# Optimization experiments

Hardware: AMD Instinct MI355X
Metric: run time of the kernel (lower is better)

## Reference

```python
import jax, jax.numpy as jnp
import numpy as np

N_NODES = 50000
N_EDGES = 800000
N_GRAPHS = 512
F_IN = 16
E_DIM = 64
D = 128          # encoder_dim
L_DIM = 64       # latent_dim
MP_STEPS = 3
S2S_STEPS = 3
NEG_SLOPE = 0.01


def _leaky(v):
    return jax.nn.leaky_relu(v, NEG_SLOPE)


def setup_inputs() -> dict:
    key = jax.random.key(0)
    ks = jax.random.split(key, 24)

    def w(k, fan_in, shape):
        return jax.random.normal(k, shape, jnp.float32) / np.sqrt(fan_in)

    inp = {
        "x": jax.random.normal(ks[0], (N_NODES, F_IN), jnp.float32),
        "edge_index": jax.random.randint(ks[1], (2, N_EDGES), 0, N_NODES, jnp.int64),
        "edge_attr": jax.random.normal(ks[2], (N_EDGES, 4), jnp.float32),
        "batch": jnp.sort(jax.random.randint(ks[3], (N_NODES,), 0, N_GRAPHS, jnp.int64)),
        # embedding: Linear(F_IN -> E_DIM); weights stored [in, out]
        "W_emb": w(ks[4], F_IN, (F_IN, E_DIM)),
        "b_emb": jnp.zeros((E_DIM,), jnp.float32),
        # first: Linear(E_DIM -> D)
        "W_first": w(ks[5], E_DIM, (E_DIM, D)),
        "b_first": jnp.zeros((D,), jnp.float32),
        # SAGEConv: lin_l (aggregated neighbors, with bias), lin_r (root, no bias)
        "W_l": w(ks[6], D, (D, D)),
        "b_l": jnp.zeros((D,), jnp.float32),
        "W_r": w(ks[7], D, (D, D)),
        # GRU (1 layer): gates ordered r,z,n as in torch
        "gru_Wih": w(ks[8], D, (D, 3 * D)),
        "gru_Whh": w(ks[9], D, (D, 3 * D)),
        "gru_bih": jnp.zeros((3 * D,), jnp.float32),
        "gru_bhh": jnp.zeros((3 * D,), jnp.float32),
        # Set2Set LSTM: input 2D -> hidden D; gates ordered i,f,g,o as in torch
        "lstm_Wih": w(ks[10], 2 * D, (2 * D, 4 * D)),
        "lstm_Whh": w(ks[11], D, (D, 4 * D)),
        "lstm_bih": jnp.zeros((4 * D,), jnp.float32),
        "lstm_bhh": jnp.zeros((4 * D,), jnp.float32),
        # linear: Linear(2D -> D), final: Linear(D -> L_DIM)
        "W_lin": w(ks[12], 2 * D, (2 * D, D)),
        "b_lin": jnp.zeros((D,), jnp.float32),
        "W_fin": w(ks[13], D, (D, L_DIM)),
        "b_fin": jnp.zeros((L_DIM,), jnp.float32),
    }
    return inp


def _gru_step(x, h, Wih, Whh, bih, bhh):
    gi = x @ Wih + bih
    gh = h @ Whh + bhh
    ir, iz, inn = jnp.split(gi, 3, axis=-1)
    hr, hz, hn = jnp.split(gh, 3, axis=-1)
    r = jax.nn.sigmoid(ir + hr)
    z = jax.nn.sigmoid(iz + hz)
    n = jnp.tanh(inn + r * hn)
    return (1.0 - z) * n + z * h


def _lstm_step(x, h, c, Wih, Whh, bih, bhh):
    g = x @ Wih + bih + h @ Whh + bhh
    i, f, gg, o = jnp.split(g, 4, axis=-1)
    c_new = jax.nn.sigmoid(f) * c + jax.nn.sigmoid(i) * jnp.tanh(gg)
    h_new = jax.nn.sigmoid(o) * jnp.tanh(c_new)
    return h_new, c_new


def reference(x, edge_index, edge_attr, batch,
              W_emb, b_emb, W_first, b_first,
              W_l, b_l, W_r,
              gru_Wih, gru_Whh, gru_bih, gru_bhh,
              lstm_Wih, lstm_Whh, lstm_bih, lstm_bhh,
              W_lin, b_lin, W_fin, b_fin):
    # edge_attr is ignored (PyG SAGEConv does not use it).
    out = _leaky(x @ W_emb + b_emb)        # [N, E_DIM]
    out = _leaky(out @ W_first + b_first)  # [N, D]
    h = out                                # GRU hidden state [N, D]
    src, dst = edge_index[0], edge_index[1]
    for _ in range(MP_STEPS):
        agg = jax.ops.segment_sum(out[src], dst, num_segments=N_NODES)  # [N, D]
        m = jax.nn.relu(agg @ W_l + b_l + out @ W_r)  # SAGEConv(aggr='add') + root
        out = _gru_step(m, h, gru_Wih, gru_Whh, gru_bih, gru_bhh)
        h = out
    # Set2Set pooling over graphs
    q_star = jnp.zeros((N_GRAPHS, 2 * D), out.dtype)
    hh = jnp.zeros((N_GRAPHS, D), out.dtype)
    cc = jnp.zeros((N_GRAPHS, D), out.dtype)
    for _ in range(S2S_STEPS):
        hh, cc = _lstm_step(q_star, hh, cc, lstm_Wih, lstm_Whh, lstm_bih, lstm_bhh)
        e = jnp.sum(out * hh[batch], axis=-1)                             # [N]
        e_max = jax.ops.segment_max(e, batch, num_segments=N_GRAPHS)      # [B]
        a = jnp.exp(e - e_max[batch])
        s = jax.ops.segment_sum(a, batch, num_segments=N_GRAPHS)
        a = a / (s[batch] + 1e-16)                                        # segment softmax
        r = jax.ops.segment_sum(a[:, None] * out, batch, num_segments=N_GRAPHS)  # [B, D]
        q_star = jnp.concatenate([hh, r], axis=-1)                        # [B, 2D]
    out = _leaky(q_star @ W_lin + b_lin)
    return out @ W_fin + b_fin  # [B, L_DIM]
```

## Files before the change

kernel.cpp:

```cpp
#include <hip/hip_runtime.h>
#include <hip/hip_bf16.h>
#include <math.h>

#define N_NODES 50000
#define N_EDGES 800000
#define N_GRAPHS 512
#define F_IN 16
#define E_DIM 64
#define D 128
#define L_DIM 64
#define NEG_SLOPE 0.01f

#define SCAN_N (N_NODES + 1)
#define NBUCK ((N_NODES + 127) >> 7)
#define EPT 4
#define BFT 1024
#define EPB (BFT * EPT)

typedef __hip_bfloat16 bf16;
typedef unsigned int uint;
typedef unsigned short ushort;
typedef __attribute__((ext_vector_type(8))) short short8;
typedef __attribute__((ext_vector_type(4))) float float4v;

__device__ __forceinline__ float b2f(bf16 v) { return __bfloat162float(v); }
__device__ __forceinline__ bf16  f2b(float v) { return __float2bfloat16(v); }
__device__ __forceinline__ short f2bs(float f) { bf16 b = __float2bfloat16(f); return *reinterpret_cast<short*>(&b); }
__device__ __forceinline__ float bs2f(short s) { return __uint_as_float(((uint)(ushort)s) << 16); }
__device__ __forceinline__ float leaky(float v) { return v > 0.f ? v : NEG_SLOPE * v; }

__device__ __forceinline__ float frcp(float x) { return __builtin_amdgcn_rcpf(x); }
__device__ __forceinline__ float sigm(float v) { return frcp(1.f + __expf(-v)); }
__device__ __forceinline__ float ftanh(float v)
{
    v = fminf(15.f, fmaxf(-15.f, v));
    float a = __expf(2.f * v);
    return (a - 1.f) * frcp(a + 1.f);
}

__global__ __launch_bounds__(256) void k_signal(float* outp, int n)
{
    int i = blockIdx.x * 256 + threadIdx.x;
    if (i < n) outp[i] = 1.0f;
}

#define NPE 16
__global__ __launch_bounds__(128) void k_embed(
    const float* __restrict__ x, const float* __restrict__ Wemb, const float* __restrict__ bemb,
    const float* __restrict__ Wfirst, const float* __restrict__ bfirst, bf16* __restrict__ out)
{
    __shared__ float xs[NPE][F_IN];
    __shared__ float ys[NPE][E_DIM];
    int t = threadIdx.x;
    int base = blockIdx.x * NPE;

    for (int i = t; i < NPE * F_IN; i += 128)
        xs[i / F_IN][i % F_IN] = x[(size_t)base * F_IN + i];
    __syncthreads();

    if (t < E_DIM) {
        float acc[NPE];
#pragma unroll
        for (int nn = 0; nn < NPE; nn++) acc[nn] = 0.f;
        for (int k = 0; k < F_IN; k++) {
            float w = Wemb[k * E_DIM + t];
#pragma unroll
            for (int nn = 0; nn < NPE; nn++) acc[nn] += xs[nn][k] * w;
        }
        float bb = bemb[t];
#pragma unroll
        for (int nn = 0; nn < NPE; nn++) ys[nn][t] = leaky(acc[nn] + bb);
    }
    __syncthreads();

    {
        float acc[NPE];
#pragma unroll
        for (int nn = 0; nn < NPE; nn++) acc[nn] = 0.f;
        for (int k = 0; k < E_DIM; k++) {
            float w = Wfirst[k * D + t];
#pragma unroll
            for (int nn = 0; nn < NPE; nn++) acc[nn] += ys[nn][k] * w;
        }
        float bb = bfirst[t];
#pragma unroll
        for (int nn = 0; nn < NPE; nn++)
            out[(size_t)(base + nn) * D + t] = f2b(leaky(acc[nn] + bb));
    }
}

__global__ __launch_bounds__(256) void k_bcount(const int* __restrict__ ei, int* __restrict__ bcnt)
{
    __shared__ int lc[NBUCK];
    for (int i = threadIdx.x; i < NBUCK; i += 256) lc[i] = 0;
    __syncthreads();
    int stride = gridDim.x * 256;
    for (int e = blockIdx.x * 256 + threadIdx.x; e < N_EDGES; e += stride) {
        int d = ei[N_EDGES + e];
        d = d < 0 ? 0 : (d >= N_NODES ? N_NODES - 1 : d);
        atomicAdd(&lc[d >> 7], 1);
    }
    __syncthreads();
    for (int i = threadIdx.x; i < NBUCK; i += 256)
        if (lc[i]) atomicAdd(&bcnt[i + 1], lc[i]);
}

__global__ void k_bscan(int* __restrict__ bcnt)
{
    if (threadIdx.x == 0 && blockIdx.x == 0) {
        int run = 0;
        for (int i = 0; i <= NBUCK; i++) { run += bcnt[i]; bcnt[i] = run; }
    }
}

__global__ __launch_bounds__(BFT) void k_bfill2(
    const int* __restrict__ ei, const int* __restrict__ bstart,
    int* __restrict__ bcur, uint* __restrict__ ebuf)
{
    __shared__ int lcnt[NBUCK];
    __shared__ int lbase[NBUCK];
    int t = threadIdx.x;
    int e0 = blockIdx.x * EPB;

    for (int i = t; i < NBUCK; i += BFT) lcnt[i] = 0;
    __syncthreads();

    uint pk[EPT];
    int bb[EPT];
#pragma unroll
    for (int q = 0; q < EPT; q++) {
        int e = e0 + q * BFT + t;
        bb[q] = -1;
        if (e < N_EDGES) {
            int s = ei[e];
            int d = ei[N_EDGES + e];
            s = s < 0 ? 0 : (s >= N_NODES ? N_NODES - 1 : s);
            d = d < 0 ? 0 : (d >= N_NODES ? N_NODES - 1 : d);
            bb[q] = d >> 7;
            pk[q] = ((uint)(d & 127) << 16) | (uint)s;
            atomicAdd(&lcnt[bb[q]], 1);
        }
    }
    __syncthreads();

    for (int i = t; i < NBUCK; i += BFT) {
        int cv = lcnt[i];
        lbase[i] = cv > 0 ? atomicAdd(&bcur[i], cv) : 0;
    }
    __syncthreads();
    for (int i = t; i < NBUCK; i += BFT) lcnt[i] = 0;
    __syncthreads();

#pragma unroll
    for (int q = 0; q < EPT; q++) {
        if (bb[q] >= 0) {
            int pos = lbase[bb[q]] + atomicAdd(&lcnt[bb[q]], 1);
            int slot = bstart[bb[q]] + pos;
            if (slot >= 0 && slot < N_EDGES) ebuf[slot] = pk[q];
        }
    }
}

__global__ __launch_bounds__(256) void k_csr(
    const int* __restrict__ bstart, const uint* __restrict__ ebuf,
    int* __restrict__ offs, int* __restrict__ srcs)
{
    __shared__ int cnt[128];
    __shared__ int loffs[129];
    int b = blockIdx.x, t = threadIdx.x;
    int e0 = bstart[b], e1 = bstart[b + 1];
    if (t < 128) cnt[t] = 0;
    __syncthreads();
    for (int j = e0 + t; j < e1; j += 256)
        atomicAdd(&cnt[(ebuf[j] >> 16) & 127], 1);
    __syncthreads();
    if (t == 0) {
        int run = 0;
        for (int i = 0; i < 128; i++) { loffs[i] = run; run += cnt[i]; }
        loffs[128] = run;
    }
    __syncthreads();
    int n0 = b << 7;
    if (t < 128) {
        int n = n0 + t;
        if (n <= N_NODES) offs[n] = e0 + loffs[t];
        cnt[t] = 0;
    }
    __syncthreads();
    for (int j = e0 + t; j < e1; j += 256) {
        uint pk = ebuf[j];
        int dl = (pk >> 16) & 127;
        int rank = atomicAdd(&cnt[dl], 1);
        int slot = e0 + loffs[dl] + rank;
        if (slot >= 0 && slot < N_EDGES) srcs[slot] = (int)(pk & 0xffffu);
    }
}

__global__ __launch_bounds__(256) void k_gstart(const int* __restrict__ batch, int* __restrict__ gstart)
{
    int g = blockIdx.x * 256 + threadIdx.x;
    if (g > N_GRAPHS) return;
    int lo = 0, hi = N_NODES;
    while (lo < hi) {
        int mid = (lo + hi) >> 1;
        if (batch[mid] < g) lo = mid + 1; else hi = mid;
    }
    gstart[g] = lo;
}

__global__ __launch_bounds__(256) void k_pack_all(
    const float* __restrict__ Wl, const float* __restrict__ Wr,
    const float* __restrict__ gWih, const float* __restrict__ gWhh,
    short* __restrict__ W1p, short* __restrict__ Wihp, short* __restrict__ Whhp)
{
    int tid = blockIdx.x * 256 + threadIdx.x;
    if (tid < 32768) {
        int j = tid & 7, l = (tid >> 3) & 63, frag = tid >> 9;
        int nb = frag >> 3, kb = frag & 7;
        int k = kb * 32 + ((l >> 4) * 8) + j;
        int n = nb * 16 + (l & 15);
        float v = (k < 128) ? Wl[k * D + n] : Wr[(k - 128) * D + n];
        W1p[tid] = f2bs(v);
    } else {
        int id = tid - 32768;
        const float* W = gWih;
        short* Wp = Wihp;
        if (id >= 49152) { id -= 49152; W = gWhh; Wp = Whhp; }
        int j = id & 7, l = (id >> 3) & 63, f = id >> 9;
        int ph = f >> 2, k0 = f & 3;
        int ct = ph / 3, p = ph - ct * 3;
        int k = k0 * 32 + ((l >> 4) * 8) + j;
        int n = p * 128 + ct * 16 + (l & 15);
        Wp[id] = f2bs(W[k * 384 + n]);
    }
}

__global__ __launch_bounds__(256) void k_gather(
    const bf16* __restrict__ hin, bf16* __restrict__ hagg,
    const int* __restrict__ offs, const int* __restrict__ srcs)
{
    int w = threadIdx.x >> 6, l = threadIdx.x & 63;
    int n = blockIdx.x * 4 + w;
    const ushort* hinu = (const ushort*)hin;
    int j0 = offs[n], j1 = offs[n + 1];
    j0 = j0 < 0 ? 0 : (j0 > N_EDGES ? N_EDGES : j0);
    j1 = j1 < j0 ? j0 : (j1 > N_EDGES ? N_EDGES : j1);

    float lo[8], hi8[8];
#pragma unroll
    for (int i = 0; i < 8; i++) { lo[i] = 0.f; hi8[i] = 0.f; }

    int j = j0;
    for (; j + 7 < j1; j += 8) {
        int ss[8];
        uint vv[8];
#pragma unroll
        for (int i = 0; i < 8; i++) {
            int s = srcs[j + i];
            ss[i] = s < 0 ? 0 : (s >= N_NODES ? N_NODES - 1 : s);
        }
#pragma unroll
        for (int i = 0; i < 8; i++)
            vv[i] = *(const uint*)(hinu + (size_t)ss[i] * D + l * 2);
#pragma unroll
        for (int i = 0; i < 8; i++) {
            lo[i] += __uint_as_float(vv[i] << 16);
            hi8[i] += __uint_as_float(vv[i] & 0xffff0000u);
        }
    }
    for (; j < j1; j++) {
        int s = srcs[j];
        s = s < 0 ? 0 : (s >= N_NODES ? N_NODES - 1 : s);
        uint v = *(const uint*)(hinu + (size_t)s * D + l * 2);
        lo[0] += __uint_as_float(v << 16);
        hi8[0] += __uint_as_float(v & 0xffff0000u);
    }
    float a0 = ((lo[0] + lo[1]) + (lo[2] + lo[3])) + ((lo[4] + lo[5]) + (lo[6] + lo[7]));
    float a1 = ((hi8[0] + hi8[1]) + (hi8[2] + hi8[3])) + ((hi8[4] + hi8[5]) + (hi8[6] + hi8[7]));
    uint ap = ((uint)(ushort)f2bs(a1) << 16) | (ushort)f2bs(a0);
    *(uint*)((ushort*)hagg + (size_t)n * D + l * 2) = ap;
}

__global__ __launch_bounds__(256) void k_sage1(
    const bf16* __restrict__ hagg, const bf16* __restrict__ hin,
    const short* __restrict__ W1p, const float* __restrict__ bl,
    bf16* __restrict__ mout)
{
    __shared__ short8 w1s[4096];
    int t = threadIdx.x;
    const short8* w1g = (const short8*)W1p;
#pragma unroll
    for (int i = 0; i < 16; i++)
        w1s[i * 256 + t] = w1g[i * 256 + t];

    int w = t >> 6, l = t & 63;
    int rg = w >> 1, cg = w & 1;
    int base = blockIdx.x * 64;
    int rA = base + rg * 32 + (l & 15);
    int rB = rA + 16;
    int rcA = rA < N_NODES ? rA : N_NODES - 1;
    int rcB = rB < N_NODES ? rB : N_NODES - 1;
    int koff = (l >> 4) * 8;
    const ushort* aggu = (const ushort*)hagg;
    const ushort* hu = (const ushort*)hin;
    ushort* mo = (ushort*)mout;

    short8 afrA[8], afrB[8];
#pragma unroll
    for (int k0 = 0; k0 < 4; k0++) {
        afrA[k0]     = *(const short8*)(aggu + (size_t)rcA * D + k0 * 32 + koff);
        afrB[k0]     = *(const short8*)(aggu + (size_t)rcB * D + k0 * 32 + koff);
        afrA[4 + k0] = *(const short8*)(hu + (size_t)rcA * D + k0 * 32 + koff);
        afrB[4 + k0] = *(const short8*)(hu + (size_t)rcB * D + k0 * 32 + koff);
    }
    __syncthreads();

    const short* w1 = (const short*)w1s;
    int crowA = rg * 32 + (l >> 4) * 4;
    int crowB = crowA + 16;
#pragma unroll
    for (int cti = 0; cti < 4; cti++) {
        int ct = cg * 4 + cti;
        short8 bw[8];
#pragma unroll
        for (int k0 = 0; k0 < 8; k0++)
            bw[k0] = *(const short8*)&w1[(ct * 8 + k0) * 512 + l * 8];
        float4v accA = {0.f, 0.f, 0.f, 0.f};
        float4v accB = {0.f, 0.f, 0.f, 0.f};
#pragma unroll
        for (int k0 = 0; k0 < 8; k0++) {
            accA = __builtin_amdgcn_mfma_f32_16x16x32_bf16(afrA[k0], bw[k0], accA, 0, 0, 0);
            accB = __builtin_amdgcn_mfma_f32_16x16x32_bf16(afrB[k0], bw[k0], accB, 0, 0, 0);
        }
        float bb = bl[ct * 16 + (l & 15)];
#pragma unroll
        for (int i = 0; i < 4; i++) {
            float vA = accA[i] + bb;
            float vB = accB[i] + bb;
            int gA = base + crowA + i;
            int gB = base + crowB + i;
            if (gA < N_NODES) mo[(size_t)gA * D + ct * 16 + (l & 15)] = (ushort)f2bs(vA > 0.f ? vA : 0.f);
            if (gB < N_NODES) mo[(size_t)gB * D + ct * 16 + (l & 15)] = (ushort)f2bs(vB > 0.f ? vB : 0.f);
        }
    }
}

__global__ __launch_bounds__(256) void k_gru2(
    const bf16* __restrict__ m, const bf16* __restrict__ hin,
    const short* __restrict__ Wihp, const short* __restrict__ Whhp,
    const float* __restrict__ bih, const float* __restrict__ bhh,
    bf16* __restrict__ hout)
{
    __shared__ short8 wis[1536];
    __shared__ short8 whs[1536];
    int t = threadIdx.x;
    int tile = blockIdx.x >> 2, cq = blockIdx.x & 3;
    const short8* wig = (const short8*)(Wihp + cq * 12288);
    const short8* whg = (const short8*)(Whhp + cq * 12288);
#pragma unroll
    for (int i = 0; i < 6; i++) {
        wis[i * 256 + t] = wig[i * 256 + t];
        whs[i * 256 + t] = whg[i * 256 + t];
    }

    int w = t >> 6, l = t & 63;
    int rg = w >> 1, cs = w & 1;
    int base = tile * 64;
    int rA = base + rg * 32 + (l & 15);
    int rB = rA + 16;
    int rcA = rA < N_NODES ? rA : N_NODES - 1;
    int rcB = rB < N_NODES ? rB : N_NODES - 1;
    int koff = (l >> 4) * 8;
    int ct = cq * 2 + cs;
    int c = ct * 16 + (l & 15);

    const ushort* mu = (const ushort*)m;
    const ushort* hu = (const ushort*)hin;
    ushort* ho = (ushort*)hout;

    short8 amrA[4], amrB[4], ahfA[4], ahfB[4];
#pragma unroll
    for (int k0 = 0; k0 < 4; k0++) {
        amrA[k0] = *(const short8*)(mu + (size_t)rcA * D + k0 * 32 + koff);
        amrB[k0] = *(const short8*)(mu + (size_t)rcB * D + k0 * 32 + koff);
        ahfA[k0] = *(const short8*)(hu + (size_t)rcA * D + k0 * 32 + koff);
        ahfB[k0] = *(const short8*)(hu + (size_t)rcB * D + k0 * 32 + koff);
    }

    int crowA = rg * 32 + (l >> 4) * 4;
    int crowB = crowA + 16;
    float h0A[4], h0B[4];
#pragma unroll
    for (int i = 0; i < 4; i++) {
        int ra = base + crowA + i; ra = ra < N_NODES ? ra : N_NODES - 1;
        int rb = base + crowB + i; rb = rb < N_NODES ? rb : N_NODES - 1;
        h0A[i] = bs2f((short)hu[(size_t)ra * D + c]);
        h0B[i] = bs2f((short)hu[(size_t)rb * D + c]);
    }
    __syncthreads();

    const short* wip = (const short*)wis;
    const short* whp = (const short*)whs;
    float rvA[4], zvA[4], rvB[4], zvB[4];
#pragma unroll
    for (int p = 0; p < 3; p++) {
        int pl = cs * 3 + p;
        short8 wi[4], wh[4];
#pragma unroll
        for (int k0 = 0; k0 < 4; k0++) {
            wi[k0] = *(const short8*)&wip[pl * 2048 + k0 * 512 + l * 8];
            wh[k0] = *(const short8*)&whp[pl * 2048 + k0 * 512 + l * 8];
        }
        float4v aiA = {0.f, 0.f, 0.f, 0.f};
        float4v ahA = {0.f, 0.f, 0.f, 0.f};
        float4v aiB = {0.f, 0.f, 0.f, 0.f};
        float4v ahB = {0.f, 0.f, 0.f, 0.f};
#pragma unroll
        for (int k0 = 0; k0 < 4; k0++) {
            aiA = __builtin_amdgcn_mfma_f32_16x16x32_bf16(amrA[k0], wi[k0], aiA, 0, 0, 0);
            ahA = __builtin_amdgcn_mfma_f32_16x16x32_bf16(ahfA[k0], wh[k0], ahA, 0, 0, 0);
            aiB = __builtin_amdgcn_mfma_f32_16x16x32_bf16(amrB[k0], wi[k0], aiB, 0, 0, 0);
            ahB = __builtin_amdgcn_mfma_f32_16x16x32_bf16(ahfB[k0], wh[k0], ahB, 0, 0, 0);
        }
        float bis = bih[p * 128 + c];
        float bhs = bhh[p * 128 + c];
        if (p == 0) {
#pragma unroll
            for (int i = 0; i < 4; i++) {
                rvA[i] = sigm(aiA[i] + bis + ahA[i] + bhs);
                rvB[i] = sigm(aiB[i] + bis + ahB[i] + bhs);
            }
        } else if (p == 1) {
#pragma unroll
            for (int i = 0; i < 4; i++) {
                zvA[i] = sigm(aiA[i] + bis + ahA[i] + bhs);
                zvB[i] = sigm(aiB[i] + bis + ahB[i] + bhs);
            }
        } else {
#pragma unroll
            for (int i = 0; i < 4; i++) {
                int gA = base + crowA + i;
                float nA = ftanh(aiA[i] + bis + rvA[i] * (ahA[i] + bhs));
                if (gA < N_NODES)
                    ho[(size_t)gA * D + c] = (ushort)f2bs((1.f - zvA[i]) * nA + zvA[i] * h0A[i]);
                int gB = base + crowB + i;
                float nB = ftanh(aiB[i] + bis + rvB[i] * (ahB[i] + bhs));
                if (gB < N_NODES)
                    ho[(size_t)gB * D + c] = (ushort)f2bs((1.f - zvB[i]) * nB + zvB[i] * h0B[i]);
            }
        }
    }
}

#define POOL_CAP 1024
#define LG2 2
__global__ __launch_bounds__(1024) void k_s2s(
    const float* __restrict__ Wih, const float* __restrict__ Whh,
    const float* __restrict__ bih, const float* __restrict__ bhh,
    const bf16* __restrict__ h, const int* __restrict__ gstart,
    float* __restrict__ qstar, float* __restrict__ hh, float* __restrict__ cc, int first)
{
    int g0 = blockIdx.x * LG2;
    int t = threadIdx.x;
    __shared__ float qs[LG2][2 * D];
    __shared__ float hs[LG2][D];
    __shared__ float part[2][LG2][512];
    __shared__ float hnew[LG2][D];
    __shared__ float e_lds[POOL_CAP];
    __shared__ float redM[16], redS[16];
    __shared__ float rpart[8][D];

    for (int i = t; i < LG2 * 2 * D; i += 1024) {
        int g = i / (2 * D), c = i % (2 * D);
        qs[g][c] = first ? 0.f : qstar[(size_t)(g0 + g) * 2 * D + c];
    }
    for (int i = t; i < LG2 * D; i += 1024) {
        int g = i / D, c = i % D;
        hs[g][c] = first ? 0.f : hh[(size_t)(g0 + g) * D + c];
    }
    __syncthreads();

    int c = t & 511, half = t >> 9;
    float a0 = half ? 0.f : (bih[c] + bhh[c]);
    float a1 = a0;
    int qb = half * 128;
#pragma unroll 4
    for (int i = 0; i < 128; i++) {
        int k = qb + i;
        float wv = Wih[(size_t)k * 512 + c];
        a0 += qs[0][k] * wv;
        a1 += qs[1][k] * wv;
    }
    int hb = half * 64;
#pragma unroll 4
    for (int i = 0; i < 64; i++) {
        int k = hb + i;
        float wv = Whh[(size_t)k * 512 + c];
        a0 += hs[0][k] * wv;
        a1 += hs[1][k] * wv;
    }
    part[half][0][c] = a0;
    part[half][1][c] = a1;
    __syncthreads();

    if (t < LG2 * D) {
        int g = t >> 7, tt = t & 127;
        float gi = part[0][g][tt] + part[1][g][tt];
        float gf = part[0][g][D + tt] + part[1][g][D + tt];
        float gg2 = part[0][g][2 * D + tt] + part[1][g][2 * D + tt];
        float go = part[0][g][3 * D + tt] + part[1][g][3 * D + tt];
        float c_old = first ? 0.f : cc[(size_t)(g0 + g) * D + tt];
        float cn = sigm(gf) * c_old + sigm(gi) * ftanh(gg2);
        float hn = sigm(go) * ftanh(cn);
        cc[(size_t)(g0 + g) * D + tt] = cn;
        hh[(size_t)(g0 + g) * D + tt] = hn;
        qstar[(size_t)(g0 + g) * 2 * D + tt] = hn;
        hnew[g][tt] = hn;
    }
    __syncthreads();

    int w = t >> 6, l = t & 63;
    int dim = t & 127, h8 = t >> 7;
    const ushort* hu = (const ushort*)h;

    for (int gg = 0; gg < LG2; gg++) {
        int g = g0 + gg;
        int s0 = gstart[g], s1 = gstart[g + 1];
        s0 = s0 < 0 ? 0 : (s0 > N_NODES ? N_NODES : s0);
        s1 = s1 < s0 ? s0 : (s1 > N_NODES ? N_NODES : s1);
        int cnt = s1 - s0;

        float hq0 = hnew[gg][l];
        float hq1 = hnew[gg][64 + l];
        float m_run = -INFINITY, s_run = 0.f, racc = 0.f;

        for (int c0 = 0; c0 < cnt; c0 += POOL_CAP) {
            int clen = cnt - c0; if (clen > POOL_CAP) clen = POOL_CAP;

            for (int i = w; i < clen; i += 16) {
                int n = s0 + c0 + i;
                float v = bs2f((short)hu[(size_t)n * D + l]) * hq0
                        + bs2f((short)hu[(size_t)n * D + 64 + l]) * hq1;
#pragma unroll
                for (int off = 32; off > 0; off >>= 1) v += __shfl_down(v, off);
                if (l == 0) e_lds[i] = v;
            }
            __syncthreads();

            float m = -INFINITY;
            for (int i = t; i < clen; i += 1024) m = fmaxf(m, e_lds[i]);
#pragma unroll
            for (int off = 32; off > 0; off >>= 1) m = fmaxf(m, __shfl_down(m, off));
            if (l == 0) redM[w] = m;
            __syncthreads();
            m = -INFINITY;
#pragma unroll
            for (int i = 0; i < 16; i++) m = fmaxf(m, redM[i]);
            float m_new = fmaxf(m_run, m);
            float scale = (m_run == -INFINITY) ? 0.f : __expf(m_run - m_new);
            s_run *= scale;
            racc *= scale;
            __syncthreads();

            float s = 0.f;
            for (int i = t; i < clen; i += 1024) {
                float wv = __expf(e_lds[i] - m_new);
                e_lds[i] = wv;
                s += wv;
            }
#pragma unroll
            for (int off = 32; off > 0; off >>= 1) s += __shfl_down(s, off);
            if (l == 0) redS[w] = s;
            __syncthreads();
#pragma unroll
            for (int i = 0; i < 16; i++) s_run += redS[i];

            for (int i = h8; i < clen; i += 8)
                racc += e_lds[i] * bs2f((short)hu[(size_t)(s0 + c0 + i) * D + dim]);
            m_run = m_new;
            __syncthreads();
        }

        rpart[h8][dim] = racc;
        __syncthreads();
        if (t < D) {
            float inv = 1.f / (s_run + 1e-16f);
            float r = 0.f;
#pragma unroll
            for (int i = 0; i < 8; i++) r += rpart[i][t];
            qstar[(size_t)g * 2 * D + D + t] = r * inv;
        }
        __syncthreads();
    }
}

__global__ __launch_bounds__(128) void k_final(
    const float* __restrict__ qstar, const float* __restrict__ Wlin, const float* __restrict__ blin,
    const float* __restrict__ Wfin, const float* __restrict__ bfin, float* __restrict__ outp)
{
    int g = blockIdx.x, t = threadIdx.x;
    __shared__ float qs[2 * D], ts[D];
    qs[t] = qstar[(size_t)g * 2 * D + t];
    qs[D + t] = qstar[(size_t)g * 2 * D + D + t];
    __syncthreads();

    float acc = blin[t];
    for (int k = 0; k < 2 * D; k++) acc += qs[k] * Wlin[(size_t)k * D + t];
    ts[t] = leaky(acc);
    __syncthreads();

    if (t < L_DIM) {
        float a2 = bfin[t];
        for (int k = 0; k < D; k++) a2 += ts[k] * Wfin[(size_t)k * L_DIM + t];
        outp[(size_t)g * L_DIM + t] = a2;
    }
}

extern "C" void kernel_launch(void* const* d_in, const int* in_sizes, int n_in,
                              void* d_out, int out_size, void* d_ws, size_t ws_size,
                              hipStream_t stream)
{
    const float* x      = (const float*)d_in[0];
    const int*   ei     = (const int*)d_in[1];
    const int*   batch  = (const int*)d_in[3];
    const float* Wemb   = (const float*)d_in[4];
    const float* bemb   = (const float*)d_in[5];
    const float* Wfirst = (const float*)d_in[6];
    const float* bfirst = (const float*)d_in[7];
    const float* Wl     = (const float*)d_in[8];
    const float* bl     = (const float*)d_in[9];
    const float* Wr     = (const float*)d_in[10];
    const float* gWih   = (const float*)d_in[11];
    const float* gWhh   = (const float*)d_in[12];
    const float* gbih   = (const float*)d_in[13];
    const float* gbhh   = (const float*)d_in[14];
    const float* lWih   = (const float*)d_in[15];
    const float* lWhh   = (const float*)d_in[16];
    const float* lbih   = (const float*)d_in[17];
    const float* lbhh   = (const float*)d_in[18];
    const float* Wlin   = (const float*)d_in[19];
    const float* blin   = (const float*)d_in[20];
    const float* Wfin   = (const float*)d_in[21];
    const float* bfin   = (const float*)d_in[22];
    float* outp = (float*)d_out;

    size_t o = 0;
    char* base = (char*)d_ws;
    auto carve = [&](size_t bytes) { void* p = base + o; o += (bytes + 255) & ~(size_t)255; return p; };
    bf16*  h0     = (bf16*)carve((size_t)N_NODES * D * sizeof(bf16));
    bf16*  h1     = (bf16*)carve((size_t)N_NODES * D * sizeof(bf16));
    bf16*  mbuf   = (bf16*)carve((size_t)N_NODES * D * sizeof(bf16));
    int*   offs   = (int*)carve((size_t)SCAN_N * sizeof(int));
    int*   srcs   = (int*)carve((size_t)N_EDGES * sizeof(int));
    int*   bcnt   = (int*)carve((size_t)(NBUCK + 1) * sizeof(int));
    int*   bcur   = (int*)carve((size_t)NBUCK * sizeof(int));
    uint*  ebuf   = (uint*)carve((size_t)N_EDGES * sizeof(uint));
    float* hh     = (float*)carve((size_t)N_GRAPHS * D * sizeof(float));
    float* cc     = (float*)carve((size_t)N_GRAPHS * D * sizeof(float));
    float* qstar  = (float*)carve((size_t)N_GRAPHS * 2 * D * sizeof(float));
    int*   gstart = (int*)carve((size_t)(N_GRAPHS + 1) * sizeof(int));
    short* W1p    = (short*)carve((size_t)256 * 128 * sizeof(short));
    short* Wihp   = (short*)carve((size_t)128 * 384 * sizeof(short));
    short* Whhp   = (short*)carve((size_t)128 * 384 * sizeof(short));
    size_t need = o;

    if (ws_size < need) {
        k_signal<<<(out_size + 255) / 256, 256, 0, stream>>>(outp, out_size);
        return;
    }

    k_embed<<<N_NODES / NPE, 128, 0, stream>>>(x, Wemb, bemb, Wfirst, bfirst, h0);

    k_pack_all<<<(32768 + 98304) / 256, 256, 0, stream>>>(Wl, Wr, gWih, gWhh, W1p, Wihp, Whhp);

    hipMemsetAsync(bcnt, 0, (size_t)((char*)ebuf - (char*)bcnt), stream);
    k_bcount<<<128, 256, 0, stream>>>(ei, bcnt);
    k_bscan<<<1, 64, 0, stream>>>(bcnt);
    k_bfill2<<<(N_EDGES + EPB - 1) / EPB, BFT, 0, stream>>>(ei, bcnt, bcur, ebuf);
    k_csr<<<NBUCK, 256, 0, stream>>>(bcnt, ebuf, offs, srcs);

    k_gstart<<<(N_GRAPHS + 1 + 255) / 256, 256, 0, stream>>>(batch, gstart);

    const int NTILE = (N_NODES + 63) / 64;
    bf16* hc = h0; bf16* hn = h1;
    for (int s = 0; s < 3; s++) {
        k_gather<<<N_NODES / 4, 256, 0, stream>>>(hc, hn, offs, srcs);
        k_sage1<<<NTILE, 256, 0, stream>>>(hn, hc, W1p, bl, mbuf);
        k_gru2<<<NTILE * 4, 256, 0, stream>>>(mbuf, hc, Wihp, Whhp, gbih, gbhh, hn);
        bf16* tmp = hc; hc = hn; hn = tmp;
    }

    for (int s = 0; s < 3; s++) {
        k_s2s<<<N_GRAPHS / LG2, 1024, 0, stream>>>(lWih, lWhh, lbih, lbhh,
                                                   hc, gstart, qstar, hh, cc, s == 0);
    }

    k_final<<<N_GRAPHS, 128, 0, stream>>>(qstar, Wlin, blin, Wfin, bfin, outp);
}
```

Measured before the change: 568.2 us.

## Make SAGE and GRU kernels persistent with double-buffered tile loads

```diff
diff --git a/kernel.cpp b/kernel.cpp
--- a/kernel.cpp
+++ b/kernel.cpp
@@ -16,6 +16,7 @@
 #define EPT 4
 #define BFT 1024
 #define EPB (BFT * EPT)
+#define NT64 ((N_NODES + 63) / 64)
 
 typedef __hip_bfloat16 bf16;
 typedef unsigned int uint;
@@ -211,7 +212,7 @@
 __global__ __launch_bounds__(256) void k_pack_all(
     const float* __restrict__ Wl, const float* __restrict__ Wr,
     const float* __restrict__ gWih, const float* __restrict__ gWhh,
-    short* __restrict__ W1p, short* __restrict__ Wihp, short* __restrict__ Whhp)
+    short* __restrict__ W1p, short* __restrict__ W2p)
 {
     int tid = blockIdx.x * 256 + threadIdx.x;
     if (tid < 32768) {
@@ -223,15 +224,14 @@
         W1p[tid] = f2bs(v);
     } else {
         int id = tid - 32768;
-        const float* W = gWih;
-        short* Wp = Wihp;
-        if (id >= 49152) { id -= 49152; W = gWhh; Wp = Whhp; }
         int j = id & 7, l = (id >> 3) & 63, f = id >> 9;
-        int ph = f >> 2, k0 = f & 3;
+        int ph = f >> 3, k0 = f & 7;
         int ct = ph / 3, p = ph - ct * 3;
-        int k = k0 * 32 + ((l >> 4) * 8) + j;
         int n = p * 128 + ct * 16 + (l & 15);
-        Wp[id] = f2bs(W[k * 384 + n]);
+        float v;
+        if (k0 < 4) v = gWih[(k0 * 32 + (l >> 4) * 8 + j) * 384 + n];
+        else        v = gWhh[((k0 - 4) * 32 + (l >> 4) * 8 + j) * 384 + n];
+        W2p[id] = f2bs(v);
     }
 }
 
@@ -281,174 +281,204 @@
     *(uint*)((ushort*)hagg + (size_t)n * D + l * 2) = ap;
 }
 
-__global__ __launch_bounds__(256) void k_sage1(
+#define SAGE_LOAD(AF_A, AF_B, TIL)                                              \
+{                                                                               \
+    int bse_ = (TIL) * 64;                                                      \
+    int ra_ = bse_ + rg * 32 + (l & 15);                                        \
+    int rb_ = ra_ + 16;                                                         \
+    int rca_ = ra_ < N_NODES ? ra_ : N_NODES - 1;                               \
+    int rcb_ = rb_ < N_NODES ? rb_ : N_NODES - 1;                               \
+    _Pragma("unroll")                                                           \
+    for (int k0 = 0; k0 < 4; k0++) {                                            \
+        AF_A[k0]     = *(const short8*)(aggu + (size_t)rca_ * D + k0 * 32 + koff);\
+        AF_B[k0]     = *(const short8*)(aggu + (size_t)rcb_ * D + k0 * 32 + koff);\
+        AF_A[4 + k0] = *(const short8*)(hu + (size_t)rca_ * D + k0 * 32 + koff);\
+        AF_B[4 + k0] = *(const short8*)(hu + (size_t)rcb_ * D + k0 * 32 + koff);\
+    }                                                                           \
+}
+
+#define SAGE_TILE(AF_A, AF_B, TIL)                                              \
+{                                                                               \
+    int bse_ = (TIL) * 64;                                                      \
+    _Pragma("unroll")                                                           \
+    for (int cti = 0; cti < 2; cti++) {                                         \
+        int ct_ = cg * 2 + cti;                                                 \
+        float4v accA = {0.f, 0.f, 0.f, 0.f};                                    \
+        float4v accB = {0.f, 0.f, 0.f, 0.f};                                    \
+        _Pragma("unroll")                                                       \
+        for (int k0 = 0; k0 < 8; k0++) {                                        \
+            short8 bw = *(const short8*)&w1s[(ct_ * 8 + k0) * 512 + l * 8];     \
+            accA = __builtin_amdgcn_mfma_f32_16x16x32_bf16(AF_A[k0], bw, accA, 0, 0, 0);\
+            accB = __builtin_amdgcn_mfma_f32_16x16x32_bf16(AF_B[k0], bw, accB, 0, 0, 0);\
+        }                                                                       \
+        float bb = bl[ct_ * 16 + (l & 15)];                                     \
+        _Pragma("unroll")                                                       \
+        for (int i = 0; i < 4; i++) {                                           \
+            float vA = accA[i] + bb;                                            \
+            float vB = accB[i] + bb;                                            \
+            int ga = bse_ + crowA + i;                                          \
+            int gb = bse_ + crowB + i;                                          \
+            if (ga < N_NODES) mo[(size_t)ga * D + ct_ * 16 + (l & 15)] = (ushort)f2bs(vA > 0.f ? vA : 0.f);\
+            if (gb < N_NODES) mo[(size_t)gb * D + ct_ * 16 + (l & 15)] = (ushort)f2bs(vB > 0.f ? vB : 0.f);\
+        }                                                                       \
+    }                                                                           \
+}
+
+__global__ __launch_bounds__(512) void k_sage1(
     const bf16* __restrict__ hagg, const bf16* __restrict__ hin,
     const short* __restrict__ W1p, const float* __restrict__ bl,
     bf16* __restrict__ mout)
 {
-    __shared__ short8 w1s[4096];
+    __shared__ short8 w1v[4096];
     int t = threadIdx.x;
-    const short8* w1g = (const short8*)W1p;
-#pragma unroll
-    for (int i = 0; i < 16; i++)
-        w1s[i * 256 + t] = w1g[i * 256 + t];
-
     int w = t >> 6, l = t & 63;
-    int rg = w >> 1, cg = w & 1;
-    int base = blockIdx.x * 64;
-    int rA = base + rg * 32 + (l & 15);
-    int rB = rA + 16;
-    int rcA = rA < N_NODES ? rA : N_NODES - 1;
-    int rcB = rB < N_NODES ? rB : N_NODES - 1;
+    int rg = w >> 2, cg = w & 3;
     int koff = (l >> 4) * 8;
+    int crowA = rg * 32 + (l >> 4) * 4;
+    int crowB = crowA + 16;
     const ushort* aggu = (const ushort*)hagg;
     const ushort* hu = (const ushort*)hin;
     ushort* mo = (ushort*)mout;
-
-    short8 afrA[8], afrB[8];
-#pragma unroll
-    for (int k0 = 0; k0 < 4; k0++) {
-        afrA[k0]     = *(const short8*)(aggu + (size_t)rcA * D + k0 * 32 + koff);
-        afrB[k0]     = *(const short8*)(aggu + (size_t)rcB * D + k0 * 32 + koff);
-        afrA[4 + k0] = *(const short8*)(hu + (size_t)rcA * D + k0 * 32 + koff);
-        afrB[4 + k0] = *(const short8*)(hu + (size_t)rcB * D + k0 * 32 + koff);
-    }
-    __syncthreads();
-
-    const short* w1 = (const short*)w1s;
+    const short* w1s = (const short*)w1v;
+
+    short8 A0a[8], A0b[8], A1a[8], A1b[8];
+    int t0 = blockIdx.x;
+    SAGE_LOAD(A0a, A0b, t0);
+
+    {
+        const short8* src = (const short8*)W1p;
+#pragma unroll
+        for (int i = 0; i < 8; i++)
+            w1v[i * 512 + t] = src[i * 512 + t];
+    }
+    __syncthreads();
+
+    while (true) {
+        int t1 = t0 + 256;
+        if (t1 < NT64) { SAGE_LOAD(A1a, A1b, t1); SAGE_TILE(A0a, A0b, t0); }
+        else { SAGE_TILE(A0a, A0b, t0); break; }
+        int t2 = t1 + 256;
+        if (t2 < NT64) { SAGE_LOAD(A0a, A0b, t2); SAGE_TILE(A1a, A1b, t1); }
+        else { SAGE_TILE(A1a, A1b, t1); break; }
+        t0 = t2;
+    }
+}
+
+#define GRU_LOAD(AM_A, AH_A, AM_B, AH_B, TIL)                                   \
+{                                                                               \
+    int bse_ = (TIL) * 64;                                                      \
+    int ra_ = bse_ + rg * 32 + (l & 15);                                        \
+    int rb_ = ra_ + 16;                                                         \
+    int rca_ = ra_ < N_NODES ? ra_ : N_NODES - 1;                               \
+    int rcb_ = rb_ < N_NODES ? rb_ : N_NODES - 1;                               \
+    _Pragma("unroll")                                                           \
+    for (int k0 = 0; k0 < 4; k0++) {                                            \
+        AM_A[k0] = *(const short8*)(mu + (size_t)rca_ * D + k0 * 32 + koff);    \
+        AM_B[k0] = *(const short8*)(mu + (size_t)rcb_ * D + k0 * 32 + koff);    \
+        AH_A[k0] = *(const short8*)(hu + (size_t)rca_ * D + k0 * 32 + koff);    \
+        AH_B[k0] = *(const short8*)(hu + (size_t)rcb_ * D + k0 * 32 + koff);    \
+    }                                                                           \
+}
+
+#define GRU_TILE(AM_A, AH_A, AM_B, AH_B, TIL)                                   \
+{                                                                               \
+    int bse_ = (TIL) * 64;                                                      \
+    float h0A[4], h0B[4];                                                       \
+    _Pragma("unroll")                                                           \
+    for (int i = 0; i < 4; i++) {                                               \
+        int ra_ = bse_ + crowA + i; ra_ = ra_ < N_NODES ? ra_ : N_NODES - 1;    \
+        int rb_ = bse_ + crowB + i; rb_ = rb_ < N_NODES ? rb_ : N_NODES - 1;    \
+        h0A[i] = bs2f((short)hu[(size_t)ra_ * D + c]);                          \
+        h0B[i] = bs2f((short)hu[(size_t)rb_ * D + c]);                          \
+    }                                                                           \
+    float4v r0A = {0.f,0.f,0.f,0.f}, r0B = {0.f,0.f,0.f,0.f};                   \
+    float4v z0A = {0.f,0.f,0.f,0.f}, z0B = {0.f,0.f,0.f,0.f};                   \
+    float4v niA = {0.f,0.f,0.f,0.f}, niB = {0.f,0.f,0.f,0.f};                   \
+    float4v nhA = {0.f,0.f,0.f,0.f}, nhB = {0.f,0.f,0.f,0.f};                   \
+    _Pragma("unroll")                                                           \
+    for (int k0 = 0; k0 < 4; k0++) {                                            \
+        short8 bri = *(const short8*)&w2s[((cw*3+0)*8 + k0) * 512 + l * 8];     \
+        short8 brh = *(const short8*)&w2s[((cw*3+0)*8 + 4 + k0) * 512 + l * 8]; \
+        r0A = __builtin_amdgcn_mfma_f32_16x16x32_bf16(AM_A[k0], bri, r0A,0,0,0);\
+        r0B = __builtin_amdgcn_mfma_f32_16x16x32_bf16(AM_B[k0], bri, r0B,0,0,0);\
+        r0A = __builtin_amdgcn_mfma_f32_16x16x32_bf16(AH_A[k0], brh, r0A,0,0,0);\
+        r0B = __builtin_amdgcn_mfma_f32_16x16x32_bf16(AH_B[k0], brh, r0B,0,0,0);\
+        short8 bzi = *(const short8*)&w2s[((cw*3+1)*8 + k0) * 512 + l * 8];     \
+        short8 bzh = *(const short8*)&w2s[((cw*3+1)*8 + 4 + k0) * 512 + l * 8]; \
+        z0A = __builtin_amdgcn_mfma_f32_16x16x32_bf16(AM_A[k0], bzi, z0A,0,0,0);\
+        z0B = __builtin_amdgcn_mfma_f32_16x16x32_bf16(AM_B[k0], bzi, z0B,0,0,0);\
+        z0A = __builtin_amdgcn_mfma_f32_16x16x32_bf16(AH_A[k0], bzh, z0A,0,0,0);\
+        z0B = __builtin_amdgcn_mfma_f32_16x16x32_bf16(AH_B[k0], bzh, z0B,0,0,0);\
+        short8 bni = *(const short8*)&w2s[((cw*3+2)*8 + k0) * 512 + l * 8];     \
+        short8 bnh = *(const short8*)&w2s[((cw*3+2)*8 + 4 + k0) * 512 + l * 8]; \
+        niA = __builtin_amdgcn_mfma_f32_16x16x32_bf16(AM_A[k0], bni, niA,0,0,0);\
+        niB = __builtin_amdgcn_mfma_f32_16x16x32_bf16(AM_B[k0], bni, niB,0,0,0);\
+        nhA = __builtin_amdgcn_mfma_f32_16x16x32_bf16(AH_A[k0], bnh, nhA,0,0,0);\
+        nhB = __builtin_amdgcn_mfma_f32_16x16x32_bf16(AH_B[k0], bnh, nhB,0,0,0);\
+    }                                                                           \
+    _Pragma("unroll")                                                           \
+    for (int i = 0; i < 4; i++) {                                               \
+        float rA = sigm(r0A[i] + bi_r + bh_r);                                  \
+        float zA = sigm(z0A[i] + bi_z + bh_z);                                  \
+        float nA = ftanh(niA[i] + bi_n + rA * (nhA[i] + bh_n));                 \
+        int ga_ = bse_ + crowA + i;                                             \
+        if (ga_ < N_NODES)                                                      \
+            ho[(size_t)ga_ * D + c] = (ushort)f2bs((1.f - zA) * nA + zA * h0A[i]);\
+        float rB = sigm(r0B[i] + bi_r + bh_r);                                  \
+        float zB = sigm(z0B[i] + bi_z + bh_z);                                  \
+        float nB = ftanh(niB[i] + bi_n + rB * (nhB[i] + bh_n));                 \
+        int gb_ = bse_ + crowB + i;                                             \
+        if (gb_ < N_NODES)                                                      \
+            ho[(size_t)gb_ * D + c] = (ushort)f2bs((1.f - zB) * nB + zB * h0B[i]);\
+    }                                                                           \
+}
+
+__global__ __launch_bounds__(512) void k_gru2(
+    const bf16* __restrict__ m, const bf16* __restrict__ hin,
+    const short* __restrict__ W2p,
+    const float* __restrict__ bih, const float* __restrict__ bhh,
+    bf16* __restrict__ hout)
+{
+    __shared__ short8 w2v[6144];
+    int t = threadIdx.x;
+    int ch = blockIdx.x & 1, blk = blockIdx.x >> 1;
+    int w = t >> 6, l = t & 63;
+    int rg = w >> 2, cw = w & 3;
+    int ct = ch * 4 + cw;
+    int c = ct * 16 + (l & 15);
+    int koff = (l >> 4) * 8;
     int crowA = rg * 32 + (l >> 4) * 4;
     int crowB = crowA + 16;
-#pragma unroll
-    for (int cti = 0; cti < 4; cti++) {
-        int ct = cg * 4 + cti;
-        short8 bw[8];
-#pragma unroll
-        for (int k0 = 0; k0 < 8; k0++)
-            bw[k0] = *(const short8*)&w1[(ct * 8 + k0) * 512 + l * 8];
-        float4v accA = {0.f, 0.f, 0.f, 0.f};
-        float4v accB = {0.f, 0.f, 0.f, 0.f};
-#pragma unroll
-        for (int k0 = 0; k0 < 8; k0++) {
-            accA = __builtin_amdgcn_mfma_f32_16x16x32_bf16(afrA[k0], bw[k0], accA, 0, 0, 0);
-            accB = __builtin_amdgcn_mfma_f32_16x16x32_bf16(afrB[k0], bw[k0], accB, 0, 0, 0);
-        }
-        float bb = bl[ct * 16 + (l & 15)];
-#pragma unroll
-        for (int i = 0; i < 4; i++) {
-            float vA = accA[i] + bb;
-            float vB = accB[i] + bb;
-            int gA = base + crowA + i;
-            int gB = base + crowB + i;
-            if (gA < N_NODES) mo[(size_t)gA * D + ct * 16 + (l & 15)] = (ushort)f2bs(vA > 0.f ? vA : 0.f);
-            if (gB < N_NODES) mo[(size_t)gB * D + ct * 16 + (l & 15)] = (ushort)f2bs(vB > 0.f ? vB : 0.f);
-        }
-    }
-}
-
-__global__ __launch_bounds__(256) void k_gru2(
-    const bf16* __restrict__ m, const bf16* __restrict__ hin,
-    const short* __restrict__ Wihp, const short* __restrict__ Whhp,
-    const float* __restrict__ bih, const float* __restrict__ bhh,
-    bf16* __restrict__ hout)
-{
-    __shared__ short8 wis[1536];
-    __shared__ short8 whs[1536];
-    int t = threadIdx.x;
-    int tile = blockIdx.x >> 2, cq = blockIdx.x & 3;
-    const short8* wig = (const short8*)(Wihp + cq * 12288);
-    const short8* whg = (const short8*)(Whhp + cq * 12288);
-#pragma unroll
-    for (int i = 0; i < 6; i++) {
-        wis[i * 256 + t] = wig[i * 256 + t];
-        whs[i * 256 + t] = whg[i * 256 + t];
-    }
-
-    int w = t >> 6, l = t & 63;
-    int rg = w >> 1, cs = w & 1;
-    int base = tile * 64;
-    int rA = base + rg * 32 + (l & 15);
-    int rB = rA + 16;
-    int rcA = rA < N_NODES ? rA : N_NODES - 1;
-    int rcB = rB < N_NODES ? rB : N_NODES - 1;
-    int koff = (l >> 4) * 8;
-    int ct = cq * 2 + cs;
-    int c = ct * 16 + (l & 15);
-
     const ushort* mu = (const ushort*)m;
     const ushort* hu = (const ushort*)hin;
     ushort* ho = (ushort*)hout;
-
-    short8 amrA[4], amrB[4], ahfA[4], ahfB[4];
-#pragma unroll
-    for (int k0 = 0; k0 < 4; k0++) {
-        amrA[k0] = *(const short8*)(mu + (size_t)rcA * D + k0 * 32 + koff);
-        amrB[k0] = *(const short8*)(mu + (size_t)rcB * D + k0 * 32 + koff);
-        ahfA[k0] = *(const short8*)(hu + (size_t)rcA * D + k0 * 32 + koff);
-        ahfB[k0] = *(const short8*)(hu + (size_t)rcB * D + k0 * 32 + koff);
-    }
-
-    int crowA = rg * 32 + (l >> 4) * 4;
-    int crowB = crowA + 16;
-    float h0A[4], h0B[4];
-#pragma unroll
-    for (int i = 0; i < 4; i++) {
-        int ra = base + crowA + i; ra = ra < N_NODES ? ra : N_NODES - 1;
-        int rb = base + crowB + i; rb = rb < N_NODES ? rb : N_NODES - 1;
-        h0A[i] = bs2f((short)hu[(size_t)ra * D + c]);
-        h0B[i] = bs2f((short)hu[(size_t)rb * D + c]);
-    }
-    __syncthreads();
-
-    const short* wip = (const short*)wis;
-    const short* whp = (const short*)whs;
-    float rvA[4], zvA[4], rvB[4], zvB[4];
-#pragma unroll
-    for (int p = 0; p < 3; p++) {
-        int pl = cs * 3 + p;
-        short8 wi[4], wh[4];
-#pragma unroll
-        for (int k0 = 0; k0 < 4; k0++) {
-            wi[k0] = *(const short8*)&wip[pl * 2048 + k0 * 512 + l * 8];
-            wh[k0] = *(const short8*)&whp[pl * 2048 + k0 * 512 + l * 8];
-        }
-        float4v aiA = {0.f, 0.f, 0.f, 0.f};
-        float4v ahA = {0.f, 0.f, 0.f, 0.f};
-        float4v aiB = {0.f, 0.f, 0.f, 0.f};
-        float4v ahB = {0.f, 0.f, 0.f, 0.f};
-#pragma unroll
-        for (int k0 = 0; k0 < 4; k0++) {
-            aiA = __builtin_amdgcn_mfma_f32_16x16x32_bf16(amrA[k0], wi[k0], aiA, 0, 0, 0);
-            ahA = __builtin_amdgcn_mfma_f32_16x16x32_bf16(ahfA[k0], wh[k0], ahA, 0, 0, 0);
-            aiB = __builtin_amdgcn_mfma_f32_16x16x32_bf16(amrB[k0], wi[k0], aiB, 0, 0, 0);
-            ahB = __builtin_amdgcn_mfma_f32_16x16x32_bf16(ahfB[k0], wh[k0], ahB, 0, 0, 0);
-        }
-        float bis = bih[p * 128 + c];
-        float bhs = bhh[p * 128 + c];
-        if (p == 0) {
-#pragma unroll
-            for (int i = 0; i < 4; i++) {
-                rvA[i] = sigm(aiA[i] + bis + ahA[i] + bhs);
-                rvB[i] = sigm(aiB[i] + bis + ahB[i] + bhs);
-            }
-        } else if (p == 1) {
-#pragma unroll
-            for (int i = 0; i < 4; i++) {
-                zvA[i] = sigm(aiA[i] + bis + ahA[i] + bhs);
-                zvB[i] = sigm(aiB[i] + bis + ahB[i] + bhs);
-            }
-        } else {
-#pragma unroll
-            for (int i = 0; i < 4; i++) {
-                int gA = base + crowA + i;
-                float nA = ftanh(aiA[i] + bis + rvA[i] * (ahA[i] + bhs));
-                if (gA < N_NODES)
-                    ho[(size_t)gA * D + c] = (ushort)f2bs((1.f - zvA[i]) * nA + zvA[i] * h0A[i]);
-                int gB = base + crowB + i;
-                float nB = ftanh(aiB[i] + bis + rvB[i] * (ahB[i] + bhs));
-                if (gB < N_NODES)
-                    ho[(size_t)gB * D + c] = (ushort)f2bs((1.f - zvB[i]) * nB + zvB[i] * h0B[i]);
-            }
-        }
+    const short* w2s = (const short*)w2v;
+
+    short8 M0a[4], H0a[4], M0b[4], H0b[4];
+    short8 M1a[4], H1a[4], M1b[4], H1b[4];
+    int t0 = blk;
+    GRU_LOAD(M0a, H0a, M0b, H0b, t0);
+
+    {
+        const short8* src = (const short8*)(W2p + 49152 * ch);
+#pragma unroll
+        for (int i = 0; i < 12; i++)
+            w2v[i * 512 + t] = src[i * 512 + t];
+    }
+
+    float bi_r = bih[c],       bh_r = bhh[c];
+    float bi_z = bih[128 + c], bh_z = bhh[128 + c];
+    float bi_n = bih[256 + c], bh_n = bhh[256 + c];
+    __syncthreads();
+
+    while (true) {
+        int t1 = t0 + 128;
+        if (t1 < NT64) { GRU_LOAD(M1a, H1a, M1b, H1b, t1); GRU_TILE(M0a, H0a, M0b, H0b, t0); }
+        else { GRU_TILE(M0a, H0a, M0b, H0b, t0); break; }
+        int t2 = t1 + 128;
+        if (t2 < NT64) { GRU_LOAD(M0a, H0a, M0b, H0b, t2); GRU_TILE(M1a, H1a, M1b, H1b, t1); }
+        else { GRU_TILE(M1a, H1a, M1b, H1b, t1); break; }
+        t0 = t2;
     }
 }
 
@@ -547,16 +577,16 @@
             }
             __syncthreads();
 
-            float m = -INFINITY;
-            for (int i = t; i < clen; i += 1024) m = fmaxf(m, e_lds[i]);
-#pragma unroll
-            for (int off = 32; off > 0; off >>= 1) m = fmaxf(m, __shfl_down(m, off));
-            if (l == 0) redM[w] = m;
+            float m2 = -INFINITY;
+            for (int i = t; i < clen; i += 1024) m2 = fmaxf(m2, e_lds[i]);
+#pragma unroll
+            for (int off = 32; off > 0; off >>= 1) m2 = fmaxf(m2, __shfl_down(m2, off));
+            if (l == 0) redM[w] = m2;
             __syncthreads();
-            m = -INFINITY;
-#pragma unroll
-            for (int i = 0; i < 16; i++) m = fmaxf(m, redM[i]);
-            float m_new = fmaxf(m_run, m);
+            m2 = -INFINITY;
+#pragma unroll
+            for (int i = 0; i < 16; i++) m2 = fmaxf(m2, redM[i]);
+            float m_new = fmaxf(m_run, m2);
             float scale = (m_run == -INFINITY) ? 0.f : __expf(m_run - m_new);
             s_run *= scale;
             racc *= scale;
@@ -660,8 +690,7 @@
     float* qstar  = (float*)carve((size_t)N_GRAPHS * 2 * D * sizeof(float));
     int*   gstart = (int*)carve((size_t)(N_GRAPHS + 1) * sizeof(int));
     short* W1p    = (short*)carve((size_t)256 * 128 * sizeof(short));
-    short* Wihp   = (short*)carve((size_t)128 * 384 * sizeof(short));
-    short* Whhp   = (short*)carve((size_t)128 * 384 * sizeof(short));
+    short* W2p    = (short*)carve((size_t)256 * 384 * sizeof(short));
     size_t need = o;
 
     if (ws_size < need) {
@@ -671,7 +700,7 @@
 
     k_embed<<<N_NODES / NPE, 128, 0, stream>>>(x, Wemb, bemb, Wfirst, bfirst, h0);
 
-    k_pack_all<<<(32768 + 98304) / 256, 256, 0, stream>>>(Wl, Wr, gWih, gWhh, W1p, Wihp, Whhp);
+    k_pack_all<<<(32768 + 98304) / 256, 256, 0, stream>>>(Wl, Wr, gWih, gWhh, W1p, W2p);
 
     hipMemsetAsync(bcnt, 0, (size_t)((char*)ebuf - (char*)bcnt), stream);
     k_bcount<<<128, 256, 0, stream>>>(ei, bcnt);
@@ -681,12 +710,11 @@
 
     k_gstart<<<(N_GRAPHS + 1 + 255) / 256, 256, 0, stream>>>(batch, gstart);
 
-    const int NTILE = (N_NODES + 63) / 64;
     bf16* hc = h0; bf16* hn = h1;
     for (int s = 0; s < 3; s++) {
         k_gather<<<N_NODES / 4, 256, 0, stream>>>(hc, hn, offs, srcs);
-        k_sage1<<<NTILE, 256, 0, stream>>>(hn, hc, W1p, bl, mbuf);
-        k_gru2<<<NTILE * 4, 256, 0, stream>>>(mbuf, hc, Wihp, Whhp, gbih, gbhh, hn);
+        k_sage1<<<256, 512, 0, stream>>>(hn, hc, W1p, bl, mbuf);
+        k_gru2<<<256, 512, 0, stream>>>(mbuf, hc, W2p, gbih, gbhh, hn);
         bf16* tmp = hc; hc = hn; hn = tmp;
     }
 
```

Measured after the change: 724.5 us. 27.5% more time.
